# Performance work log

Hardware: AMD Instinct MI355X
Metric: run time of the kernel (lower is better)

The kernel has to match this reference:

```python
import jax, jax.numpy as jnp
import numpy as np

DIM = 192
HEADS = 6
HEAD_DIM = DIM // HEADS          # 32
N_WIN_TOK = 2 * 6 * 12           # 144 tokens per (2,6,12) window
BIAS_ROWS = (2 * 12 - 1) * 6 * 6 * 2 * 2  # 3312
N_WINDOWS = 960


def setup_inputs() -> dict:
    key = jax.random.key(0)
    ks = jax.random.split(key, 8)
    x = jax.random.normal(ks[0], (N_WINDOWS, N_WIN_TOK, DIM), dtype=jnp.float32)
    mask = jax.random.randint(ks[1], (N_WINDOWS, N_WIN_TOK, N_WIN_TOK), 0, 2, dtype=jnp.int32)
    rel_index = jax.random.randint(ks[2], (N_WIN_TOK, N_WIN_TOK), 0, BIAS_ROWS, dtype=jnp.int32)
    # parameters (torch nn.Linear equivalents, stored as [in, out])
    w_qkv = jax.random.normal(ks[3], (DIM, 3 * DIM), dtype=jnp.float32) * 0.02
    b_qkv = jnp.zeros((3 * DIM,), dtype=jnp.float32)
    w_out = jax.random.normal(ks[4], (DIM, DIM), dtype=jnp.float32) * 0.02
    b_out = jnp.zeros((DIM,), dtype=jnp.float32)
    bias_table = jax.random.normal(ks[5], (BIAS_ROWS, HEADS), dtype=jnp.float32) * 0.02
    return {"x": x, "mask": mask, "rel_index": rel_index,
            "w_qkv": w_qkv, "b_qkv": b_qkv, "w_out": w_out, "b_out": b_out,
            "bias_table": bias_table}


def reference(x, mask, rel_index, w_qkv, b_qkv, w_out, b_out, bias_table):
    nW, N, dim = x.shape
    scale = jnp.asarray(HEAD_DIM, x.dtype) ** -0.5
    # qkv projection: [nW, N, 3, heads, head_dim]
    qkv = (x @ w_qkv + b_qkv).reshape(nW, N, 3, HEADS, HEAD_DIM)
    q, k, v = qkv[:, :, 0], qkv[:, :, 1], qkv[:, :, 2]   # each [nW, N, heads, hd]
    # attention scores [nW, heads, N, N]
    attn = jnp.einsum('wnhd,wmhd->whnm', q * scale, k)
    # relative-position bias gather: table[rel_index] -> [N, N, heads] -> [heads, N, N]
    bias = bias_table[rel_index].transpose(2, 0, 1)
    attn = attn + bias[None]
    # additive mask: positions where mask == 0 get -1e9
    attn = jnp.where(mask[:, None, :, :] == 0, jnp.asarray(-1e9, attn.dtype), attn)
    attn = jax.nn.softmax(attn, axis=-1)
    out = jnp.einsum('whnm,wmhd->wnhd', attn, v).reshape(nW, N, dim)
    return out @ w_out + b_out
```

## Files before the change

kernel.cpp:

```cpp
#include <hip/hip_runtime.h>
#include <math.h>

#define NW 960
#define NT 144
#define DIM 192
#define NH 6
#define HD 32
#define WCOLS 576

typedef __bf16 bf16x8 __attribute__((ext_vector_type(8)));
typedef float floatx4 __attribute__((ext_vector_type(4)));

__device__ __forceinline__ unsigned short f2bf(float x) {
    union { float f; unsigned u; } v; v.f = x;
    unsigned r = v.u + 0x7fffu + ((v.u >> 16) & 1u);
    return (unsigned short)(r >> 16);
}
__device__ __forceinline__ float bf2f(unsigned short b) {
    union { unsigned u; float f; } v; v.u = ((unsigned)b) << 16;
    return v.f;
}
__device__ __forceinline__ floatx4 mfma16(bf16x8 a, bf16x8 b, floatx4 c) {
    return __builtin_amdgcn_mfma_f32_16x16x32_bf16(a, b, c, 0, 0, 0);
}
__device__ __forceinline__ bf16x8 lds_ld8(const unsigned short* p) {
    bf16x8 v;
    __builtin_memcpy(&v, p, 16);
    return v;
}

__global__ void prep_bias(const int* __restrict__ rel_index,
                          const float* __restrict__ bias_table,
                          float* __restrict__ bias_pre) {
    int i = blockIdx.x * 256 + threadIdx.x;
    if (i < NH * NT * NT) {
        int h = i / (NT * NT);
        int rem = i - h * (NT * NT);
        bias_pre[i] = bias_table[rel_index[rem] * NH + h];
    }
}

__global__ void prep_wq_frag(const float* __restrict__ w_qkv,
                             unsigned short* __restrict__ wh,
                             unsigned short* __restrict__ wl) {
    int i = blockIdx.x * 256 + threadIdx.x;
    if (i < NH * 6 * 6 * 512) {
        int h = i / 18432; int r = i - h * 18432;
        int j = r / 3072;  r -= j * 3072;
        int kt = r / 512;  r -= kt * 512;
        int lane = r >> 3, pos = r & 7;
        int col96 = j * 16 + (lane & 15);
        int k = kt * 32 + (lane >> 4) * 8 + pos;
        float v = w_qkv[k * WCOLS + (col96 >> 5) * DIM + h * HD + (col96 & 31)];
        unsigned short hi = f2bf(v);
        wh[i] = hi;
        wl[i] = f2bf(v - bf2f(hi));
    }
}

__global__ void prep_wo_frag(const float* __restrict__ w_out,
                             unsigned short* __restrict__ wh,
                             unsigned short* __restrict__ wl) {
    int i = blockIdx.x * 256 + threadIdx.x;
    if (i < 12 * 6 * 512) {
        int nt = i / 3072; int r = i - nt * 3072;
        int kt = r / 512;  r -= kt * 512;
        int lane = r >> 3, pos = r & 7;
        int ocol = nt * 16 + (lane & 15);
        int k = kt * 32 + (lane >> 4) * 8 + pos;
        float v = w_out[k * DIM + ocol];
        unsigned short hi = f2bf(v);
        wh[i] = hi;
        wl[i] = f2bf(v - bf2f(hi));
    }
}

__global__ __launch_bounds__(384, 1)
void fused(const float* __restrict__ x, const int* __restrict__ mask,
           const float* __restrict__ bias_pre,
           const unsigned short* __restrict__ wqh, const unsigned short* __restrict__ wql,
           const float* __restrict__ b_qkv,
           const unsigned short* __restrict__ woh_g, const unsigned short* __restrict__ wol_g,
           const float* __restrict__ b_out, float* __restrict__ out)
{
    __shared__ __align__(16) unsigned short lds[73120];
    const int XFo = 0, Q2o = 27648, K2o = 36864, V2o = 46080, Po = 56320, MBo = 71680;

    const int t = threadIdx.x;
    const int w = blockIdx.x;
    const int lane = t & 63, wv = t >> 6;
    const int c = lane & 15, q = lane >> 4;
    const float scale = 0.17677669529663687f;
    const float* xg = x + (size_t)w * NT * DIM;

    {
        unsigned* XFd = (unsigned*)&lds[XFo];
        #pragma unroll
        for (int l = 0; l < 36; ++l) {
            int d = t + l * 384;
            int kt = d / 2304; int r2 = d - kt * 2304;
            int tile = r2 >> 8; int r3 = r2 & 255;
            int ln = r3 >> 2, pp = r3 & 3;
            int n = tile * 16 + (ln & 15);
            int k = kt * 32 + (ln >> 4) * 8 + pp * 2;
            float2 xv = *(const float2*)&xg[n * DIM + k];
            XFd[d] = (unsigned)f2bf(xv.x) | ((unsigned)f2bf(xv.y) << 16);
        }
    }
    for (int e = t; e < 2560; e += 384) {
        if (e < 1024) {
            int gi = e >> 8, l2 = 32 + ((e >> 3) & 31), pos = e & 7;
            lds[V2o + (gi * 5 + 4) * 512 + l2 * 8 + pos] = 0;
        } else {
            int e2 = e - 1024;
            int wvi = e2 >> 8, l2 = 32 + ((e2 >> 3) & 31), pos = e2 & 7;
            lds[Po + (wvi * 5 + 4) * 512 + l2 * 8 + pos] = 0;
        }
    }
    {
        unsigned* mb = (unsigned*)&lds[MBo];
        #pragma unroll 4
        for (int rr = 0; rr < 24; ++rr) {
            int n = wv * 24 + rr;
            const int* mrow = mask + ((size_t)w * NT + n) * NT;
            unsigned long long b0 = __ballot(mrow[lane] != 0);
            unsigned long long b1 = __ballot(mrow[64 + lane] != 0);
            int mv = (lane < 16) ? mrow[128 + lane] : 0;
            unsigned long long b2 = __ballot(mv != 0);
            if (lane == 0) {
                mb[n * 5 + 0] = (unsigned)b0;
                mb[n * 5 + 1] = (unsigned)(b0 >> 32);
                mb[n * 5 + 2] = (unsigned)b1;
                mb[n * 5 + 3] = (unsigned)(b1 >> 32);
                mb[n * 5 + 4] = (unsigned)b2;
            }
        }
    }

    const int part = wv % 3;
    const int hlA  = wv / 3;
    const int j0   = part * 2;
    const int hlB  = wv & 1;
    const int s0   = wv >> 1;

    floatx4 Oacc[3][3][2];

    #pragma unroll
    for (int g = 0; g < 3; ++g) {
        __syncthreads();
        const int hg = 2 * g + hlA;

        const unsigned short* bh0p = wqh + (size_t)((hg * 6 + j0) * 6) * 512 + lane * 8;
        const unsigned short* bh1p = wqh + (size_t)((hg * 6 + j0 + 1) * 6) * 512 + lane * 8;
        const unsigned short* bl0p = wql + (size_t)((hg * 6 + j0) * 6) * 512 + lane * 8;
        const unsigned short* bl1p = wql + (size_t)((hg * 6 + j0 + 1) * 6) * 512 + lane * 8;
        bf16x8 bh0[6], bh1[6], bl0a[6], bl1a[6];
        #pragma unroll
        for (int kt = 0; kt < 6; ++kt) {
            bh0[kt]  = *(const bf16x8*)&bh0p[kt * 512];
            bh1[kt]  = *(const bf16x8*)&bh1p[kt * 512];
            bl0a[kt] = *(const bf16x8*)&bl0p[kt * 512];
            bl1a[kt] = *(const bf16x8*)&bl1p[kt * 512];
        }
        float bq0 = b_qkv[part * DIM + hg * HD + c];
        float bq1 = b_qkv[part * DIM + hg * HD + 16 + c];

        #pragma unroll
        for (int i3 = 0; i3 < 3; ++i3) {
            floatx4 a[3][2];
            #pragma unroll
            for (int ii = 0; ii < 3; ++ii) { a[ii][0] = (floatx4)0.0f; a[ii][1] = (floatx4)0.0f; }
            __builtin_amdgcn_s_setprio(1);
            #pragma unroll
            for (int kt = 0; kt < 6; ++kt) {
                #pragma unroll
                for (int ii = 0; ii < 3; ++ii) {
                    bf16x8 ah = *(const bf16x8*)&lds[XFo + (kt * 9 + i3 * 3 + ii) * 512 + lane * 8];
                    a[ii][0] = mfma16(ah, bh0[kt], a[ii][0]);
                    a[ii][0] = mfma16(ah, bl0a[kt], a[ii][0]);
                    a[ii][1] = mfma16(ah, bh1[kt], a[ii][1]);
                    a[ii][1] = mfma16(ah, bl1a[kt], a[ii][1]);
                }
            }
            __builtin_amdgcn_s_setprio(0);
            #pragma unroll
            for (int ii = 0; ii < 3; ++ii) {
                int i = i3 * 3 + ii;
                #pragma unroll
                for (int r = 0; r < 4; ++r) {
                    float v0 = a[ii][0][r] + bq0;
                    float v1 = a[ii][1][r] + bq1;
                    if (part == 0) {
                        lds[Q2o + (hlA * 9 + i) * 512 + ((q * 4 + r) + 16 * (c >> 3)) * 8 + (c & 7)] = f2bf(v0 * scale);
                        lds[Q2o + (hlA * 9 + i) * 512 + ((q * 4 + r) + 16 * (2 + (c >> 3))) * 8 + (c & 7)] = f2bf(v1 * scale);
                    } else if (part == 1) {
                        lds[K2o + (hlA * 9 + i) * 512 + ((q * 4 + r) + 16 * (c >> 3)) * 8 + (c & 7)] = f2bf(v0);
                        lds[K2o + (hlA * 9 + i) * 512 + ((q * 4 + r) + 16 * (2 + (c >> 3))) * 8 + (c & 7)] = f2bf(v1);
                    } else {
                        int n = i * 16 + q * 4 + r;
                        lds[V2o + ((hlA * 2 + 0) * 5 + (n >> 5)) * 512 + (c + 16 * ((n >> 3) & 3)) * 8 + (n & 7)] = f2bf(v0);
                        lds[V2o + ((hlA * 2 + 1) * 5 + (n >> 5)) * 512 + (c + 16 * ((n >> 3) & 3)) * 8 + (n & 7)] = f2bf(v1);
                    }
                }
            }
        }
        __syncthreads();

        const int hB = 2 * g + hlB;
        #pragma unroll
        for (int it = 0; it < 3; ++it) {
            int s = s0 + 3 * it;
            float bb[4][9];
            const float* bbase = bias_pre + hB * (NT * NT) + (s * 16 + q * 4) * NT + c;
            #pragma unroll
            for (int r = 0; r < 4; ++r)
                #pragma unroll
                for (int nt = 0; nt < 9; ++nt)
                    bb[r][nt] = bbase[r * NT + nt * 16];
            bf16x8 qf = *(const bf16x8*)&lds[Q2o + (hlB * 9 + s) * 512 + lane * 8];
            floatx4 sacc[9];
            __builtin_amdgcn_s_setprio(1);
            #pragma unroll
            for (int nt = 0; nt < 9; ++nt) {
                bf16x8 kf = *(const bf16x8*)&lds[K2o + (hlB * 9 + nt) * 512 + lane * 8];
                sacc[nt] = mfma16(qf, kf, (floatx4)0.0f);
            }
            __builtin_amdgcn_s_setprio(0);
            const unsigned* mb = (const unsigned*)&lds[MBo];
            unsigned mwv[4][5];
            #pragma unroll
            for (int r = 0; r < 4; ++r) {
                int n = s * 16 + q * 4 + r;
                #pragma unroll
                for (int k5 = 0; k5 < 5; ++k5) mwv[r][k5] = mb[n * 5 + k5];
            }
            float e[4][9], mx[4];
            #pragma unroll
            for (int r = 0; r < 4; ++r) mx[r] = -1e30f;
            #pragma unroll
            for (int r = 0; r < 4; ++r)
                #pragma unroll
                for (int nt = 0; nt < 9; ++nt) {
                    float val = sacc[nt][r] + bb[r][nt];
                    unsigned bit = (mwv[r][nt >> 1] >> (((nt & 1) << 4) + c)) & 1u;
                    val = bit ? val : -1e9f;
                    e[r][nt] = val; mx[r] = fmaxf(mx[r], val);
                }
            #pragma unroll
            for (int o = 8; o; o >>= 1)
                #pragma unroll
                for (int r = 0; r < 4; ++r) mx[r] = fmaxf(mx[r], __shfl_xor(mx[r], o, 64));
            float sum[4] = {0.f, 0.f, 0.f, 0.f};
            #pragma unroll
            for (int r = 0; r < 4; ++r)
                #pragma unroll
                for (int nt = 0; nt < 9; ++nt) { e[r][nt] = __expf(e[r][nt] - mx[r]); sum[r] += e[r][nt]; }
            #pragma unroll
            for (int o = 8; o; o >>= 1)
                #pragma unroll
                for (int r = 0; r < 4; ++r) sum[r] += __shfl_xor(sum[r], o, 64);
            #pragma unroll
            for (int r = 0; r < 4; ++r) {
                float rinv = 1.0f / sum[r];
                #pragma unroll
                for (int nt = 0; nt < 9; ++nt) {
                    int col = nt * 16 + c;
                    lds[Po + (wv * 5 + (col >> 5)) * 512 +
                        ((q * 4 + r) + 16 * ((col >> 3) & 3)) * 8 + (col & 7)] = f2bf(e[r][nt] * rinv);
                }
            }
            asm volatile("" ::: "memory");
            floatx4 o0 = (floatx4)0.0f, o1 = (floatx4)0.0f;
            __builtin_amdgcn_s_setprio(1);
            #pragma unroll
            for (int sl = 0; sl < 5; ++sl) {
                bf16x8 pf = lds_ld8(&lds[Po + (wv * 5 + sl) * 512 + lane * 8]);
                o0 = mfma16(pf, *(const bf16x8*)&lds[V2o + ((hlB * 2 + 0) * 5 + sl) * 512 + lane * 8], o0);
                o1 = mfma16(pf, *(const bf16x8*)&lds[V2o + ((hlB * 2 + 1) * 5 + sl) * 512 + lane * 8], o1);
            }
            __builtin_amdgcn_s_setprio(0);
            Oacc[g][it][0] = o0; Oacc[g][it][1] = o1;
        }
    }

    #pragma unroll
    for (int g = 0; g < 3; ++g) {
        int hB = 2 * g + hlB;
        #pragma unroll
        for (int it = 0; it < 3; ++it) {
            int s = s0 + 3 * it;
            #pragma unroll
            for (int ntv = 0; ntv < 2; ++ntv) {
                #pragma unroll
                for (int r = 0; r < 4; ++r) {
                    lds[XFo + (hB * 9 + s) * 512 +
                        ((q * 4 + r) + 16 * (ntv * 2 + (c >> 3))) * 8 + (c & 7)] =
                        f2bf(Oacc[g][it][ntv][r]);
                }
            }
        }
    }
    __syncthreads();

    {
        const int colt0 = 2 * wv;
        const unsigned short* wh0p = woh_g + (size_t)(colt0 * 6) * 512 + lane * 8;
        const unsigned short* wh1p = woh_g + (size_t)((colt0 + 1) * 6) * 512 + lane * 8;
        const unsigned short* wl0p = wol_g + (size_t)(colt0 * 6) * 512 + lane * 8;
        const unsigned short* wl1p = wol_g + (size_t)((colt0 + 1) * 6) * 512 + lane * 8;
        bf16x8 wh0[6], wh1[6], wlo0[6], wlo1[6];
        #pragma unroll
        for (int kt = 0; kt < 6; ++kt) {
            wh0[kt]  = *(const bf16x8*)&wh0p[kt * 512];
            wh1[kt]  = *(const bf16x8*)&wh1p[kt * 512];
            wlo0[kt] = *(const bf16x8*)&wl0p[kt * 512];
            wlo1[kt] = *(const bf16x8*)&wl1p[kt * 512];
        }
        float bo0 = b_out[colt0 * 16 + c];
        float bo1 = b_out[colt0 * 16 + 16 + c];
        #pragma unroll
        for (int i3 = 0; i3 < 3; ++i3) {
            floatx4 a2[3][2];
            #pragma unroll
            for (int ii = 0; ii < 3; ++ii) { a2[ii][0] = (floatx4)0.0f; a2[ii][1] = (floatx4)0.0f; }
            __builtin_amdgcn_s_setprio(1);
            #pragma unroll
            for (int kt = 0; kt < 6; ++kt) {
                #pragma unroll
                for (int ii = 0; ii < 3; ++ii) {
                    bf16x8 af = *(const bf16x8*)&lds[XFo + (kt * 9 + i3 * 3 + ii) * 512 + lane * 8];
                    a2[ii][0] = mfma16(af, wh0[kt], a2[ii][0]);
                    a2[ii][0] = mfma16(af, wlo0[kt], a2[ii][0]);
                    a2[ii][1] = mfma16(af, wh1[kt], a2[ii][1]);
                    a2[ii][1] = mfma16(af, wlo1[kt], a2[ii][1]);
                }
            }
            __builtin_amdgcn_s_setprio(0);
            #pragma unroll
            for (int ii = 0; ii < 3; ++ii) {
                int n0 = (i3 * 3 + ii) * 16 + q * 4;
                #pragma unroll
                for (int r = 0; r < 4; ++r) {
                    size_t ro = ((size_t)w * NT + n0 + r) * DIM;
                    out[ro + colt0 * 16 + c] = a2[ii][0][r] + bo0;
                    out[ro + colt0 * 16 + 16 + c] = a2[ii][1][r] + bo1;
                }
            }
        }
    }
}

__global__ __launch_bounds__(256, 2)
void attn_kernel(const float* __restrict__ x, const int* __restrict__ mask,
                 const int* __restrict__ rel_index, const float* __restrict__ w_qkv,
                 const float* __restrict__ b_qkv, const float* __restrict__ bias_table,
                 float* __restrict__ out)
{
    __shared__ float smem[19136];
    float* xt = smem;
    float* wt = smem + 4768;
    float* qs = smem;
    float* ks = smem + 4752;
    float* vs = smem + 9504;
    float* S  = smem + 14400;

    const int t  = threadIdx.x;
    const int w  = blockIdx.x / NH;
    const int h  = blockIdx.x % NH;
    const int tx = t & 15;
    const int ty = t >> 4;
    const float scale = 0.17677669529663687f;
    const float* xg = x + (size_t)w * NT * DIM;

    float acc[9][6];
    #pragma unroll
    for (int i = 0; i < 9; ++i)
        #pragma unroll
        for (int j = 0; j < 6; ++j) acc[i][j] = 0.f;

    for (int kt = 0; kt < 6; ++kt) {
        #pragma unroll
        for (int l = 0; l < 18; ++l) {
            int e = t + l * 256;
            int n = e >> 5, kk = e & 31;
            xt[kk * 149 + n] = xg[n * DIM + kt * 32 + kk];
        }
        #pragma unroll
        for (int l = 0; l < 12; ++l) {
            int e = t + l * 256;
            int kk = e / 96, cc = e - kk * 96;
            int col = (cc >> 5) * DIM + h * HD + (cc & 31);
            wt[kk * 96 + cc] = w_qkv[(kt * 32 + kk) * WCOLS + col];
        }
        __syncthreads();
        #pragma unroll
        for (int kk = 0; kk < 32; ++kk) {
            float a[9], b[6];
            #pragma unroll
            for (int i = 0; i < 9; ++i) a[i] = xt[kk * 149 + ty * 9 + i];
            #pragma unroll
            for (int j = 0; j < 6; ++j) b[j] = wt[kk * 96 + tx * 6 + j];
            #pragma unroll
            for (int i = 0; i < 9; ++i)
                #pragma unroll
                for (int j = 0; j < 6; ++j) acc[i][j] = fmaf(a[i], b[j], acc[i][j]);
        }
        __syncthreads();
    }

    #pragma unroll
    for (int j = 0; j < 6; ++j) {
        int cc = tx * 6 + j;
        int part = cc >> 5, jj = cc & 31;
        float bq = b_qkv[part * DIM + h * HD + jj];
        #pragma unroll
        for (int i = 0; i < 9; ++i) {
            int r = ty * 9 + i;
            float val = acc[i][j] + bq;
            if (part == 0)      qs[r * 33 + jj] = val * scale;
            else if (part == 1) ks[r * 33 + jj] = val;
            else                vs[r * 34 + jj] = val;
        }
    }
    __syncthreads();

    const int wave = t >> 6, lane = t & 63;
    for (int rt = 0; rt < 5; ++rt) {
        const int rows = (rt == 4) ? 16 : 32;
        {
            int r0 = ty * 2;
            int n0 = rt * 32 + r0; if (n0 > NT - 1) n0 = NT - 1;
            int n1 = n0 + 1;       if (n1 > NT - 1) n1 = NT - 1;
            int m0 = tx * 9;
            float s0[9], s1[9];
            #pragma unroll
            for (int j = 0; j < 9; ++j) { s0[j] = 0.f; s1[j] = 0.f; }
            #pragma unroll
            for (int kk = 0; kk < 32; ++kk) {
                float a0 = qs[n0 * 33 + kk];
                float a1 = qs[n1 * 33 + kk];
                #pragma unroll
                for (int j = 0; j < 9; ++j) {
                    float bk = ks[(m0 + j) * 33 + kk];
                    s0[j] = fmaf(a0, bk, s0[j]);
                    s1[j] = fmaf(a1, bk, s1[j]);
                }
            }
            if (r0 < rows) {
                #pragma unroll
                for (int j = 0; j < 9; ++j) S[r0 * 148 + m0 + j] = s0[j];
                #pragma unroll
                for (int j = 0; j < 9; ++j) S[(r0 + 1) * 148 + m0 + j] = s1[j];
            }
        }
        __syncthreads();

        for (int r = wave; r < rows; r += 4) {
            int n = rt * 32 + r;
            const int* mrow = mask + ((size_t)w * NT + n) * NT;
            const int* rrow = rel_index + n * NT;
            float e0 = S[r * 148 + lane] + bias_table[rrow[lane] * NH + h];
            if (mrow[lane] == 0) e0 = -1e9f;
            float e1 = S[r * 148 + 64 + lane] + bias_table[rrow[64 + lane] * NH + h];
            if (mrow[64 + lane] == 0) e1 = -1e9f;
            float e2 = -INFINITY;
            if (lane < 16) {
                e2 = S[r * 148 + 128 + lane] + bias_table[rrow[128 + lane] * NH + h];
                if (mrow[128 + lane] == 0) e2 = -1e9f;
            }
            float vmax = fmaxf(fmaxf(e0, e1), e2);
            #pragma unroll
            for (int off = 32; off > 0; off >>= 1)
                vmax = fmaxf(vmax, __shfl_xor(vmax, off, 64));
            float p0 = __expf(e0 - vmax);
            float p1 = __expf(e1 - vmax);
            float p2 = (lane < 16) ? __expf(e2 - vmax) : 0.f;
            float s = p0 + p1 + p2;
            #pragma unroll
            for (int off = 32; off > 0; off >>= 1)
                s += __shfl_xor(s, off, 64);
            float rinv = 1.f / s;
            S[r * 148 + lane] = p0 * rinv;
            S[r * 148 + 64 + lane] = p1 * rinv;
            if (lane < 16) S[r * 148 + 128 + lane] = p2 * rinv;
        }
        __syncthreads();

        {
            int r0 = ty * 2, dd0 = tx * 2;
            if (r0 < rows) {
                float o00 = 0, o01 = 0, o10 = 0, o11 = 0;
                #pragma unroll
                for (int m = 0; m < NT; ++m) {
                    float p0 = S[r0 * 148 + m];
                    float p1 = S[(r0 + 1) * 148 + m];
                    float2 vv = *(const float2*)&vs[m * 34 + dd0];
                    o00 = fmaf(p0, vv.x, o00);
                    o01 = fmaf(p0, vv.y, o01);
                    o10 = fmaf(p1, vv.x, o10);
                    o11 = fmaf(p1, vv.y, o11);
                }
                int n0 = rt * 32 + r0;
                *(float2*)&out[((size_t)(w * NT + n0)) * DIM + h * HD + dd0] = make_float2(o00, o01);
                *(float2*)&out[((size_t)(w * NT + n0 + 1)) * DIM + h * HD + dd0] = make_float2(o10, o11);
            }
        }
        __syncthreads();
    }
}

__global__ __launch_bounds__(256, 2)
void proj_kernel(float* __restrict__ io, const float* __restrict__ w_out,
                 const float* __restrict__ b_out)
{
    __shared__ float in_t[64 * 196];
    __shared__ float wt[32 * 192];
    const int t = threadIdx.x;
    const size_t row0 = (size_t)blockIdx.x * 64;

    #pragma unroll
    for (int l = 0; l < 12; ++l) {
        int e = t + l * 256;
        int r = e / 48, c4 = e - r * 48;
        float4 val = *(const float4*)&io[(row0 + r) * DIM + c4 * 4];
        *(float4*)&in_t[r * 196 + c4 * 4] = val;
    }
    const int tx = t & 15, ty = t >> 4;
    float acc[4][12];
    #pragma unroll
    for (int i = 0; i < 4; ++i)
        #pragma unroll
        for (int j = 0; j < 12; ++j) acc[i][j] = 0.f;

    for (int kt = 0; kt < 6; ++kt) {
        __syncthreads();
        #pragma unroll
        for (int l = 0; l < 6; ++l) {
            int e = t + l * 256;
            int kk = e / 48, c4 = e - kk * 48;
            *(float4*)&wt[kk * 192 + c4 * 4] =
                *(const float4*)&w_out[(kt * 32 + kk) * DIM + c4 * 4];
        }
        __syncthreads();
        #pragma unroll
        for (int kk = 0; kk < 32; ++kk) {
            float a[4];
            #pragma unroll
            for (int i = 0; i < 4; ++i) a[i] = in_t[(ty * 4 + i) * 196 + kt * 32 + kk];
            float b[12];
            #pragma unroll
            for (int j4 = 0; j4 < 3; ++j4) {
                float4 bb = *(const float4*)&wt[kk * 192 + tx * 12 + j4 * 4];
                b[j4 * 4] = bb.x; b[j4 * 4 + 1] = bb.y;
                b[j4 * 4 + 2] = bb.z; b[j4 * 4 + 3] = bb.w;
            }
            #pragma unroll
            for (int i = 0; i < 4; ++i)
                #pragma unroll
                for (int j = 0; j < 12; ++j)
                    acc[i][j] = fmaf(a[i], b[j], acc[i][j]);
        }
    }

    float bo[12];
    #pragma unroll
    for (int j4 = 0; j4 < 3; ++j4) {
        float4 bb = *(const float4*)&b_out[tx * 12 + j4 * 4];
        bo[j4 * 4] = bb.x; bo[j4 * 4 + 1] = bb.y;
        bo[j4 * 4 + 2] = bb.z; bo[j4 * 4 + 3] = bb.w;
    }
    #pragma unroll
    for (int i = 0; i < 4; ++i) {
        size_t r = row0 + ty * 4 + i;
        #pragma unroll
        for (int j4 = 0; j4 < 3; ++j4) {
            float4 o;
            o.x = acc[i][j4 * 4]     + bo[j4 * 4];
            o.y = acc[i][j4 * 4 + 1] + bo[j4 * 4 + 1];
            o.z = acc[i][j4 * 4 + 2] + bo[j4 * 4 + 2];
            o.w = acc[i][j4 * 4 + 3] + bo[j4 * 4 + 3];
            *(float4*)&io[r * DIM + tx * 12 + j4 * 4] = o;
        }
    }
}

extern "C" void kernel_launch(void* const* d_in, const int* in_sizes, int n_in,
                              void* d_out, int out_size, void* d_ws, size_t ws_size,
                              hipStream_t stream) {
    const float* x          = (const float*)d_in[0];
    const int*   mask       = (const int*)d_in[1];
    const int*   rel_index  = (const int*)d_in[2];
    const float* w_qkv      = (const float*)d_in[3];
    const float* b_qkv      = (const float*)d_in[4];
    const float* w_out      = (const float*)d_in[5];
    const float* b_out      = (const float*)d_in[6];
    const float* bias_table = (const float*)d_in[7];
    float* out = (float*)d_out;

    const size_t WS_NEED = 1087488;

    if (ws_size >= WS_NEED) {
        char* ws = (char*)d_ws;
        float*          bias_pre = (float*)ws;
        unsigned short* wq_h     = (unsigned short*)(ws + 497664);
        unsigned short* wq_l     = (unsigned short*)(ws + 718848);
        unsigned short* wo_h     = (unsigned short*)(ws + 940032);
        unsigned short* wo_l     = (unsigned short*)(ws + 1013760);

        hipLaunchKernelGGL(prep_bias, dim3(486), dim3(256), 0, stream,
                           rel_index, bias_table, bias_pre);
        hipLaunchKernelGGL(prep_wq_frag, dim3(432), dim3(256), 0, stream,
                           w_qkv, wq_h, wq_l);
        hipLaunchKernelGGL(prep_wo_frag, dim3(144), dim3(256), 0, stream,
                           w_out, wo_h, wo_l);
        hipLaunchKernelGGL(fused, dim3(NW), dim3(384), 0, stream,
                           x, mask, bias_pre, wq_h, wq_l, b_qkv,
                           wo_h, wo_l, b_out, out);
    } else {
        hipLaunchKernelGGL(attn_kernel, dim3(NW * NH), dim3(256), 0, stream,
                           x, mask, rel_index, w_qkv, b_qkv, bias_table, out);
        hipLaunchKernelGGL(proj_kernel, dim3(NW * NT / 64), dim3(256), 0, stream,
                           out, w_out, b_out);
    }
}
```

Measured before the change: 529.3 us.

## Double fused kernel to 12 waves and shrink P scratch to one tile per wave

The fused window kernel now runs 768 threads per block instead of 384. Each wave computes one 16-column tile of the QKV and output projections instead of two, and the attention work is split as 9 row tiles over 12 waves. The softmax P buffer drops to one 512-element tile per wave, which is written and consumed slice by slice before each PV MFMA. That frees LDS so up to three blocks can be resident per CU. The aim is more waves in flight to hide latency, at the cost of fewer registers per thread and an uneven attention load, since waves 0-5 handle two row tiles and waves 6-11 handle one.

```diff
diff --git a/kernel.cpp b/kernel.cpp
--- a/kernel.cpp
+++ b/kernel.cpp
@@ -75,7 +75,7 @@
     }
 }
 
-__global__ __launch_bounds__(384, 1)
+__global__ __launch_bounds__(768, 3)
 void fused(const float* __restrict__ x, const int* __restrict__ mask,
            const float* __restrict__ bias_pre,
            const unsigned short* __restrict__ wqh, const unsigned short* __restrict__ wql,
@@ -83,8 +83,8 @@
            const unsigned short* __restrict__ woh_g, const unsigned short* __restrict__ wol_g,
            const float* __restrict__ b_out, float* __restrict__ out)
 {
-    __shared__ __align__(16) unsigned short lds[73120];
-    const int XFo = 0, Q2o = 27648, K2o = 36864, V2o = 46080, Po = 56320, MBo = 71680;
+    __shared__ __align__(16) unsigned short lds[63904];
+    const int XFo = 0, Q2o = 27648, K2o = 36864, V2o = 46080, Po = 56320, MBo = 62464;
 
     const int t = threadIdx.x;
     const int w = blockIdx.x;
@@ -96,8 +96,8 @@
     {
         unsigned* XFd = (unsigned*)&lds[XFo];
         #pragma unroll
-        for (int l = 0; l < 36; ++l) {
-            int d = t + l * 384;
+        for (int l = 0; l < 18; ++l) {
+            int d = t + l * 768;
             int kt = d / 2304; int r2 = d - kt * 2304;
             int tile = r2 >> 8; int r3 = r2 & 255;
             int ln = r3 >> 2, pp = r3 & 3;
@@ -107,21 +107,15 @@
             XFd[d] = (unsigned)f2bf(xv.x) | ((unsigned)f2bf(xv.y) << 16);
         }
     }
-    for (int e = t; e < 2560; e += 384) {
-        if (e < 1024) {
-            int gi = e >> 8, l2 = 32 + ((e >> 3) & 31), pos = e & 7;
-            lds[V2o + (gi * 5 + 4) * 512 + l2 * 8 + pos] = 0;
-        } else {
-            int e2 = e - 1024;
-            int wvi = e2 >> 8, l2 = 32 + ((e2 >> 3) & 31), pos = e2 & 7;
-            lds[Po + (wvi * 5 + 4) * 512 + l2 * 8 + pos] = 0;
-        }
+    for (int e = t; e < 1024; e += 768) {
+        int gi = e >> 8, l2 = 32 + ((e >> 3) & 31), pos = e & 7;
+        lds[V2o + (gi * 5 + 4) * 512 + l2 * 8 + pos] = 0;
     }
     {
         unsigned* mb = (unsigned*)&lds[MBo];
         #pragma unroll 4
-        for (int rr = 0; rr < 24; ++rr) {
-            int n = wv * 24 + rr;
+        for (int rr = 0; rr < 12; ++rr) {
+            int n = wv * 12 + rr;
             const int* mrow = mask + ((size_t)w * NT + n) * NT;
             unsigned long long b0 = __ballot(mrow[lane] != 0);
             unsigned long long b1 = __ballot(mrow[64 + lane] != 0);
@@ -137,49 +131,121 @@
         }
     }
 
-    const int part = wv % 3;
-    const int hlA  = wv / 3;
-    const int j0   = part * 2;
-    const int hlB  = wv & 1;
-    const int s0   = wv >> 1;
-
-    floatx4 Oacc[3][3][2];
+    const int hl   = wv / 6;
+    const int j6   = wv % 6;
+    const int part = j6 >> 1;
+    const int jj   = j6 & 1;
+    const int hl2  = wv & 1;
+    const int sA   = wv >> 1;
+
+    floatx4 Oacc[3][2][2];
+
+    auto attn_unit = [&](int g, int s, floatx4* O) {
+        const int hB = 2 * g + hl2;
+        float bb[4][9];
+        const float* bbase = bias_pre + hB * (NT * NT) + (s * 16 + q * 4) * NT + c;
+        #pragma unroll
+        for (int r = 0; r < 4; ++r)
+            #pragma unroll
+            for (int nt = 0; nt < 9; ++nt)
+                bb[r][nt] = bbase[r * NT + nt * 16];
+        bf16x8 qf = *(const bf16x8*)&lds[Q2o + (hl2 * 9 + s) * 512 + lane * 8];
+        floatx4 sacc[9];
+        __builtin_amdgcn_s_setprio(1);
+        #pragma unroll
+        for (int nt = 0; nt < 9; ++nt) {
+            bf16x8 kf = *(const bf16x8*)&lds[K2o + (hl2 * 9 + nt) * 512 + lane * 8];
+            sacc[nt] = mfma16(qf, kf, (floatx4)0.0f);
+        }
+        __builtin_amdgcn_s_setprio(0);
+        const unsigned* mb = (const unsigned*)&lds[MBo];
+        unsigned mwv[4][5];
+        #pragma unroll
+        for (int r = 0; r < 4; ++r) {
+            int n = s * 16 + q * 4 + r;
+            #pragma unroll
+            for (int k5 = 0; k5 < 5; ++k5) mwv[r][k5] = mb[n * 5 + k5];
+        }
+        float e[4][9], mx[4];
+        #pragma unroll
+        for (int r = 0; r < 4; ++r) mx[r] = -1e30f;
+        #pragma unroll
+        for (int r = 0; r < 4; ++r)
+            #pragma unroll
+            for (int nt = 0; nt < 9; ++nt) {
+                float val = sacc[nt][r] + bb[r][nt];
+                unsigned bit = (mwv[r][nt >> 1] >> (((nt & 1) << 4) + c)) & 1u;
+                val = bit ? val : -1e9f;
+                e[r][nt] = val; mx[r] = fmaxf(mx[r], val);
+            }
+        #pragma unroll
+        for (int o = 8; o; o >>= 1)
+            #pragma unroll
+            for (int r = 0; r < 4; ++r) mx[r] = fmaxf(mx[r], __shfl_xor(mx[r], o, 64));
+        float sum[4] = {0.f, 0.f, 0.f, 0.f};
+        #pragma unroll
+        for (int r = 0; r < 4; ++r)
+            #pragma unroll
+            for (int nt = 0; nt < 9; ++nt) { e[r][nt] = __expf(e[r][nt] - mx[r]); sum[r] += e[r][nt]; }
+        #pragma unroll
+        for (int o = 8; o; o >>= 1)
+            #pragma unroll
+            for (int r = 0; r < 4; ++r) sum[r] += __shfl_xor(sum[r], o, 64);
+        float rinv[4];
+        #pragma unroll
+        for (int r = 0; r < 4; ++r) rinv[r] = 1.0f / sum[r];
+        floatx4 o0 = (floatx4)0.0f, o1 = (floatx4)0.0f;
+        unsigned short* pbase = &lds[Po + wv * 512];
+        #pragma unroll
+        for (int sl = 0; sl < 5; ++sl) {
+            asm volatile("" ::: "memory");
+            #pragma unroll
+            for (int r = 0; r < 4; ++r)
+                #pragma unroll
+                for (int ntl = 0; ntl < 2; ++ntl) {
+                    int nt = 2 * sl + ntl;
+                    unsigned short pv = 0;
+                    if (nt < 9) pv = f2bf(e[r][nt] * rinv[r]);
+                    pbase[((q * 4 + r) + 16 * ((ntl << 1) + (c >> 3))) * 8 + (c & 7)] = pv;
+                }
+            asm volatile("" ::: "memory");
+            bf16x8 pf = lds_ld8(&pbase[lane * 8]);
+            __builtin_amdgcn_s_setprio(1);
+            o0 = mfma16(pf, *(const bf16x8*)&lds[V2o + ((hl2 * 2 + 0) * 5 + sl) * 512 + lane * 8], o0);
+            o1 = mfma16(pf, *(const bf16x8*)&lds[V2o + ((hl2 * 2 + 1) * 5 + sl) * 512 + lane * 8], o1);
+            __builtin_amdgcn_s_setprio(0);
+        }
+        O[0] = o0; O[1] = o1;
+    };
 
     #pragma unroll
     for (int g = 0; g < 3; ++g) {
         __syncthreads();
-        const int hg = 2 * g + hlA;
-
-        const unsigned short* bh0p = wqh + (size_t)((hg * 6 + j0) * 6) * 512 + lane * 8;
-        const unsigned short* bh1p = wqh + (size_t)((hg * 6 + j0 + 1) * 6) * 512 + lane * 8;
-        const unsigned short* bl0p = wql + (size_t)((hg * 6 + j0) * 6) * 512 + lane * 8;
-        const unsigned short* bl1p = wql + (size_t)((hg * 6 + j0 + 1) * 6) * 512 + lane * 8;
-        bf16x8 bh0[6], bh1[6], bl0a[6], bl1a[6];
+        const int hg = 2 * g + hl;
+
+        const unsigned short* bhp = wqh + (size_t)((hg * 6 + j6) * 6) * 512 + lane * 8;
+        const unsigned short* blp = wql + (size_t)((hg * 6 + j6) * 6) * 512 + lane * 8;
+        bf16x8 bh[6], bl[6];
         #pragma unroll
         for (int kt = 0; kt < 6; ++kt) {
-            bh0[kt]  = *(const bf16x8*)&bh0p[kt * 512];
-            bh1[kt]  = *(const bf16x8*)&bh1p[kt * 512];
-            bl0a[kt] = *(const bf16x8*)&bl0p[kt * 512];
-            bl1a[kt] = *(const bf16x8*)&bl1p[kt * 512];
-        }
-        float bq0 = b_qkv[part * DIM + hg * HD + c];
-        float bq1 = b_qkv[part * DIM + hg * HD + 16 + c];
+            bh[kt] = *(const bf16x8*)&bhp[kt * 512];
+            bl[kt] = *(const bf16x8*)&blp[kt * 512];
+        }
+        float bq = b_qkv[part * DIM + hg * HD + jj * 16 + c];
 
         #pragma unroll
         for (int i3 = 0; i3 < 3; ++i3) {
-            floatx4 a[3][2];
-            #pragma unroll
-            for (int ii = 0; ii < 3; ++ii) { a[ii][0] = (floatx4)0.0f; a[ii][1] = (floatx4)0.0f; }
+            floatx4 a[3];
+            #pragma unroll
+            for (int ii = 0; ii < 3; ++ii) a[ii] = (floatx4)0.0f;
             __builtin_amdgcn_s_setprio(1);
             #pragma unroll
             for (int kt = 0; kt < 6; ++kt) {
                 #pragma unroll
                 for (int ii = 0; ii < 3; ++ii) {
                     bf16x8 ah = *(const bf16x8*)&lds[XFo + (kt * 9 + i3 * 3 + ii) * 512 + lane * 8];
-                    a[ii][0] = mfma16(ah, bh0[kt], a[ii][0]);
-                    a[ii][0] = mfma16(ah, bl0a[kt], a[ii][0]);
-                    a[ii][1] = mfma16(ah, bh1[kt], a[ii][1]);
-                    a[ii][1] = mfma16(ah, bl1a[kt], a[ii][1]);
+                    a[ii] = mfma16(ah, bh[kt], a[ii]);
+                    a[ii] = mfma16(ah, bl[kt], a[ii]);
                 }
             }
             __builtin_amdgcn_s_setprio(0);
@@ -188,151 +254,70 @@
                 int i = i3 * 3 + ii;
                 #pragma unroll
                 for (int r = 0; r < 4; ++r) {
-                    float v0 = a[ii][0][r] + bq0;
-                    float v1 = a[ii][1][r] + bq1;
+                    float v = a[ii][r] + bq;
+                    int col32 = jj * 16 + c;
                     if (part == 0) {
-                        lds[Q2o + (hlA * 9 + i) * 512 + ((q * 4 + r) + 16 * (c >> 3)) * 8 + (c & 7)] = f2bf(v0 * scale);
-                        lds[Q2o + (hlA * 9 + i) * 512 + ((q * 4 + r) + 16 * (2 + (c >> 3))) * 8 + (c & 7)] = f2bf(v1 * scale);
+                        lds[Q2o + (hl * 9 + i) * 512 + ((q * 4 + r) + 16 * (col32 >> 3)) * 8 + (col32 & 7)] = f2bf(v * scale);
                     } else if (part == 1) {
-                        lds[K2o + (hlA * 9 + i) * 512 + ((q * 4 + r) + 16 * (c >> 3)) * 8 + (c & 7)] = f2bf(v0);
-                        lds[K2o + (hlA * 9 + i) * 512 + ((q * 4 + r) + 16 * (2 + (c >> 3))) * 8 + (c & 7)] = f2bf(v1);
+                        lds[K2o + (hl * 9 + i) * 512 + ((q * 4 + r) + 16 * (col32 >> 3)) * 8 + (col32 & 7)] = f2bf(v);
                     } else {
                         int n = i * 16 + q * 4 + r;
-                        lds[V2o + ((hlA * 2 + 0) * 5 + (n >> 5)) * 512 + (c + 16 * ((n >> 3) & 3)) * 8 + (n & 7)] = f2bf(v0);
-                        lds[V2o + ((hlA * 2 + 1) * 5 + (n >> 5)) * 512 + (c + 16 * ((n >> 3) & 3)) * 8 + (n & 7)] = f2bf(v1);
+                        lds[V2o + ((hl * 2 + jj) * 5 + (n >> 5)) * 512 + (c + 16 * ((n >> 3) & 3)) * 8 + (n & 7)] = f2bf(v);
                     }
                 }
             }
         }
         __syncthreads();
 
-        const int hB = 2 * g + hlB;
-        #pragma unroll
-        for (int it = 0; it < 3; ++it) {
-            int s = s0 + 3 * it;
-            float bb[4][9];
-            const float* bbase = bias_pre + hB * (NT * NT) + (s * 16 + q * 4) * NT + c;
+        attn_unit(g, sA, Oacc[g][0]);
+        if (wv < 6) attn_unit(g, 6 + sA, Oacc[g][1]);
+    }
+
+    #pragma unroll
+    for (int g = 0; g < 3; ++g) {
+        int hB = 2 * g + hl2;
+        #pragma unroll
+        for (int ntv = 0; ntv < 2; ++ntv)
             #pragma unroll
             for (int r = 0; r < 4; ++r)
-                #pragma unroll
-                for (int nt = 0; nt < 9; ++nt)
-                    bb[r][nt] = bbase[r * NT + nt * 16];
-            bf16x8 qf = *(const bf16x8*)&lds[Q2o + (hlB * 9 + s) * 512 + lane * 8];
-            floatx4 sacc[9];
-            __builtin_amdgcn_s_setprio(1);
-            #pragma unroll
-            for (int nt = 0; nt < 9; ++nt) {
-                bf16x8 kf = *(const bf16x8*)&lds[K2o + (hlB * 9 + nt) * 512 + lane * 8];
-                sacc[nt] = mfma16(qf, kf, (floatx4)0.0f);
-            }
-            __builtin_amdgcn_s_setprio(0);
-            const unsigned* mb = (const unsigned*)&lds[MBo];
-            unsigned mwv[4][5];
-            #pragma unroll
-            for (int r = 0; r < 4; ++r) {
-                int n = s * 16 + q * 4 + r;
-                #pragma unroll
-                for (int k5 = 0; k5 < 5; ++k5) mwv[r][k5] = mb[n * 5 + k5];
-            }
-            float e[4][9], mx[4];
-            #pragma unroll
-            for (int r = 0; r < 4; ++r) mx[r] = -1e30f;
-            #pragma unroll
-            for (int r = 0; r < 4; ++r)
-                #pragma unroll
-                for (int nt = 0; nt < 9; ++nt) {
-                    float val = sacc[nt][r] + bb[r][nt];
-                    unsigned bit = (mwv[r][nt >> 1] >> (((nt & 1) << 4) + c)) & 1u;
-                    val = bit ? val : -1e9f;
-                    e[r][nt] = val; mx[r] = fmaxf(mx[r], val);
-                }
-            #pragma unroll
-            for (int o = 8; o; o >>= 1)
-                #pragma unroll
-                for (int r = 0; r < 4; ++r) mx[r] = fmaxf(mx[r], __shfl_xor(mx[r], o, 64));
-            float sum[4] = {0.f, 0.f, 0.f, 0.f};
-            #pragma unroll
-            for (int r = 0; r < 4; ++r)
-                #pragma unroll
-                for (int nt = 0; nt < 9; ++nt) { e[r][nt] = __expf(e[r][nt] - mx[r]); sum[r] += e[r][nt]; }
-            #pragma unroll
-            for (int o = 8; o; o >>= 1)
-                #pragma unroll
-                for (int r = 0; r < 4; ++r) sum[r] += __shfl_xor(sum[r], o, 64);
-            #pragma unroll
-            for (int r = 0; r < 4; ++r) {
-                float rinv = 1.0f / sum[r];
-                #pragma unroll
-                for (int nt = 0; nt < 9; ++nt) {
-                    int col = nt * 16 + c;
-                    lds[Po + (wv * 5 + (col >> 5)) * 512 +
-                        ((q * 4 + r) + 16 * ((col >> 3) & 3)) * 8 + (col & 7)] = f2bf(e[r][nt] * rinv);
-                }
-            }
-            asm volatile("" ::: "memory");
-            floatx4 o0 = (floatx4)0.0f, o1 = (floatx4)0.0f;
-            __builtin_amdgcn_s_setprio(1);
-            #pragma unroll
-            for (int sl = 0; sl < 5; ++sl) {
-                bf16x8 pf = lds_ld8(&lds[Po + (wv * 5 + sl) * 512 + lane * 8]);
-                o0 = mfma16(pf, *(const bf16x8*)&lds[V2o + ((hlB * 2 + 0) * 5 + sl) * 512 + lane * 8], o0);
-                o1 = mfma16(pf, *(const bf16x8*)&lds[V2o + ((hlB * 2 + 1) * 5 + sl) * 512 + lane * 8], o1);
-            }
-            __builtin_amdgcn_s_setprio(0);
-            Oacc[g][it][0] = o0; Oacc[g][it][1] = o1;
-        }
-    }
-
-    #pragma unroll
-    for (int g = 0; g < 3; ++g) {
-        int hB = 2 * g + hlB;
-        #pragma unroll
-        for (int it = 0; it < 3; ++it) {
-            int s = s0 + 3 * it;
-            #pragma unroll
-            for (int ntv = 0; ntv < 2; ++ntv) {
-                #pragma unroll
-                for (int r = 0; r < 4; ++r) {
-                    lds[XFo + (hB * 9 + s) * 512 +
+                lds[XFo + (hB * 9 + sA) * 512 +
+                    ((q * 4 + r) + 16 * (ntv * 2 + (c >> 3))) * 8 + (c & 7)] =
+                    f2bf(Oacc[g][0][ntv][r]);
+        if (wv < 6) {
+            #pragma unroll
+            for (int ntv = 0; ntv < 2; ++ntv)
+                #pragma unroll
+                for (int r = 0; r < 4; ++r)
+                    lds[XFo + (hB * 9 + 6 + sA) * 512 +
                         ((q * 4 + r) + 16 * (ntv * 2 + (c >> 3))) * 8 + (c & 7)] =
-                        f2bf(Oacc[g][it][ntv][r]);
-                }
-            }
+                        f2bf(Oacc[g][1][ntv][r]);
         }
     }
     __syncthreads();
 
     {
-        const int colt0 = 2 * wv;
-        const unsigned short* wh0p = woh_g + (size_t)(colt0 * 6) * 512 + lane * 8;
-        const unsigned short* wh1p = woh_g + (size_t)((colt0 + 1) * 6) * 512 + lane * 8;
-        const unsigned short* wl0p = wol_g + (size_t)(colt0 * 6) * 512 + lane * 8;
-        const unsigned short* wl1p = wol_g + (size_t)((colt0 + 1) * 6) * 512 + lane * 8;
-        bf16x8 wh0[6], wh1[6], wlo0[6], wlo1[6];
+        const unsigned short* whp = woh_g + (size_t)(wv * 6) * 512 + lane * 8;
+        const unsigned short* wlp = wol_g + (size_t)(wv * 6) * 512 + lane * 8;
+        bf16x8 wh[6], wlo[6];
         #pragma unroll
         for (int kt = 0; kt < 6; ++kt) {
-            wh0[kt]  = *(const bf16x8*)&wh0p[kt * 512];
-            wh1[kt]  = *(const bf16x8*)&wh1p[kt * 512];
-            wlo0[kt] = *(const bf16x8*)&wl0p[kt * 512];
-            wlo1[kt] = *(const bf16x8*)&wl1p[kt * 512];
-        }
-        float bo0 = b_out[colt0 * 16 + c];
-        float bo1 = b_out[colt0 * 16 + 16 + c];
+            wh[kt]  = *(const bf16x8*)&whp[kt * 512];
+            wlo[kt] = *(const bf16x8*)&wlp[kt * 512];
+        }
+        float bo = b_out[wv * 16 + c];
         #pragma unroll
         for (int i3 = 0; i3 < 3; ++i3) {
-            floatx4 a2[3][2];
-            #pragma unroll
-            for (int ii = 0; ii < 3; ++ii) { a2[ii][0] = (floatx4)0.0f; a2[ii][1] = (floatx4)0.0f; }
+            floatx4 a2[3];
+            #pragma unroll
+            for (int ii = 0; ii < 3; ++ii) a2[ii] = (floatx4)0.0f;
             __builtin_amdgcn_s_setprio(1);
             #pragma unroll
             for (int kt = 0; kt < 6; ++kt) {
                 #pragma unroll
                 for (int ii = 0; ii < 3; ++ii) {
                     bf16x8 af = *(const bf16x8*)&lds[XFo + (kt * 9 + i3 * 3 + ii) * 512 + lane * 8];
-                    a2[ii][0] = mfma16(af, wh0[kt], a2[ii][0]);
-                    a2[ii][0] = mfma16(af, wlo0[kt], a2[ii][0]);
-                    a2[ii][1] = mfma16(af, wh1[kt], a2[ii][1]);
-                    a2[ii][1] = mfma16(af, wlo1[kt], a2[ii][1]);
+                    a2[ii] = mfma16(af, wh[kt], a2[ii]);
+                    a2[ii] = mfma16(af, wlo[kt], a2[ii]);
                 }
             }
             __builtin_amdgcn_s_setprio(0);
@@ -342,8 +327,7 @@
                 #pragma unroll
                 for (int r = 0; r < 4; ++r) {
                     size_t ro = ((size_t)w * NT + n0 + r) * DIM;
-                    out[ro + colt0 * 16 + c] = a2[ii][0][r] + bo0;
-                    out[ro + colt0 * 16 + 16 + c] = a2[ii][1][r] + bo1;
+                    out[ro + wv * 16 + c] = a2[ii][r] + bo;
                 }
             }
         }
@@ -613,7 +597,7 @@
                            w_qkv, wq_h, wq_l);
         hipLaunchKernelGGL(prep_wo_frag, dim3(144), dim3(256), 0, stream,
                            w_out, wo_h, wo_l);
-        hipLaunchKernelGGL(fused, dim3(NW), dim3(384), 0, stream,
+        hipLaunchKernelGGL(fused, dim3(NW), dim3(768), 0, stream,
                            x, mask, bias_pre, wq_h, wq_l, b_qkv,
                            wo_h, wo_l, b_out, out);
     } else {
```

New measurement: 496.4 us. -6.2%, faster.
